# Performance work log

Hardware: AMD Instinct MI355X
Metric: run time of the kernel (lower is better)

The kernel has to match this reference:

```python
import jax, jax.numpy as jnp
import numpy as np

B, T, D, U = 32, 2048, 1024, 1024


def setup_inputs() -> dict:
    key = jax.random.key(0)
    ks = jax.random.split(key, 6)
    scale = 0.02
    return {
        "query": jax.random.normal(ks[0], (B, D), jnp.float32),
        "values": jax.random.normal(ks[1], (B, T, D), jnp.float32),
        "W1_k": jax.random.normal(ks[2], (D, U), jnp.float32) * scale,
        "W1_b": jnp.zeros((U,), jnp.float32),
        "W2_k": jax.random.normal(ks[3], (D, U), jnp.float32) * scale,
        "W2_b": jnp.zeros((U,), jnp.float32),
        "V_k": jax.random.normal(ks[4], (U, 1), jnp.float32) * scale,
        "V_b": jnp.zeros((1,), jnp.float32),
    }


def reference(query, values, W1_k, W1_b, W2_k, W2_b, V_k, V_b):
    # query: [B, D] -> [B, 1, U]; values: [B, T, D] -> [B, T, U]
    q_proj = (query @ W1_k + W1_b)[:, None, :]
    v_proj = jnp.einsum("btd,du->btu", values, W2_k) + W2_b
    # score: [B, T, 1]
    score = jnp.tanh(q_proj + v_proj) @ V_k + V_b
    attention_weights = jax.nn.softmax(score, axis=1)  # over time axis T
    context_vector = jnp.sum(attention_weights * values, axis=1)  # [B, D]
    return context_vector
```

## Files before the change

### kernel.cpp

```cpp
#include <hip/hip_runtime.h>

#define NB 32
#define NT 2048
#define ND 1024
#define NU 1024
#define NM (NB*NT)

using f32x4 = __attribute__((ext_vector_type(4))) float;
using s16x8 = __attribute__((ext_vector_type(8))) short;

#define BAR()   asm volatile("s_barrier" ::: "memory")
#define LGKM0() asm volatile("s_waitcnt lgkmcnt(0)" ::: "memory")
#define VMC(n)  asm volatile("s_waitcnt vmcnt(" #n ")" ::: "memory")

__device__ __forceinline__ unsigned short f2bf(float f) {
  unsigned u = __builtin_bit_cast(unsigned, f);
  u = u + 0x7fffu + ((u >> 16) & 1u);
  return (unsigned short)(u >> 16);
}

__device__ __forceinline__ void gload_lds16(const void* g, void* l) {
  __builtin_amdgcn_global_load_lds(
      (const __attribute__((address_space(1))) unsigned int*)g,
      (__attribute__((address_space(3))) unsigned int*)l, 16, 0, 0);
}

__device__ __forceinline__ float tanh_fast(float x) {
  float e = __expf(2.0f * x);
  return 1.0f - 2.0f * __builtin_amdgcn_rcpf(e + 1.0f);
}

__device__ __forceinline__ void stage_half(const unsigned short* g, int gk,
                                           unsigned short* l, int w, int r3, int c8s) {
#pragma unroll
  for (int i = 0; i < 2; ++i) {
    int cb = i * 8 + w;
    gload_lds16(g + (((size_t)(cb * 8 + r3)) << 10) + gk + c8s * 8, l + cb * 512);
  }
}

#define MFMA_Q(MB, NBASE) \
  _Pragma("unroll") \
  for (int m = 0; m < 4; ++m) { \
    _Pragma("unroll") \
    for (int n = 0; n < 2; ++n) { \
      _Pragma("unroll") \
      for (int ks = 0; ks < 2; ++ks) \
        acc[(MB) + m][(NBASE) + n] = __builtin_amdgcn_mfma_f32_16x16x32_bf16( \
            fa[m][ks], fb[(NBASE) + n][ks], acc[(MB) + m][(NBASE) + n], 0, 0, 0); \
    } \
  }

template<bool S1, bool S2, bool S3, bool S4, int VMN>
__device__ __forceinline__ void tile_body(
    int kt, int buf,
    const unsigned short* __restrict__ gA, const unsigned short* __restrict__ gB,
    unsigned short* sA, unsigned short* sB, f32x4 (&acc)[8][4],
    int w, int wr, int wc, int l15, int lg, int r3, int c8s) {
  const unsigned short* pA = sA + buf * 16384;
  const unsigned short* pB = sB + buf * 16384;
  const int l7 = l15 & 7;
  s16x8 fa[4][2], fb[4][2];
#pragma unroll
  for (int m = 0; m < 4; ++m)
#pragma unroll
    for (int ks = 0; ks < 2; ++ks)
      fa[m][ks] = *(const s16x8*)(pA + ((wr * 128 + m * 16 + l15) << 6) + (((ks * 4 + lg) ^ l7) << 3));
#pragma unroll
  for (int n = 0; n < 4; ++n)
#pragma unroll
    for (int ks = 0; ks < 2; ++ks)
      fb[n][ks] = *(const s16x8*)(pB + ((wc * 64 + n * 16 + l15) << 6) + (((ks * 4 + lg) ^ l7) << 3));
  if (S1) stage_half(gA + (128 << 10), (kt + 1) * 64, sA + (buf ^ 1) * 16384 + 8192, w, r3, c8s);
  BAR(); LGKM0(); __builtin_amdgcn_sched_barrier(0);
  __builtin_amdgcn_s_setprio(1);
  MFMA_Q(0, 0);
  __builtin_amdgcn_s_setprio(0);
  BAR();
  if (S2) stage_half(gB, (kt + 2) * 64, sB + buf * 16384, w, r3, c8s);
  BAR();
  __builtin_amdgcn_s_setprio(1);
  MFMA_Q(0, 2);
  __builtin_amdgcn_s_setprio(0);
  BAR();
#pragma unroll
  for (int m = 0; m < 4; ++m)
#pragma unroll
    for (int ks = 0; ks < 2; ++ks)
      fa[m][ks] = *(const s16x8*)(pA + ((wr * 128 + (4 + m) * 16 + l15) << 6) + (((ks * 4 + lg) ^ l7) << 3));
  if (S3) stage_half(gB + (128 << 10), (kt + 2) * 64, sB + buf * 16384 + 8192, w, r3, c8s);
  BAR(); LGKM0(); __builtin_amdgcn_sched_barrier(0);
  __builtin_amdgcn_s_setprio(1);
  MFMA_Q(4, 0);
  __builtin_amdgcn_s_setprio(0);
  BAR();
  if (S4) stage_half(gA, (kt + 2) * 64, sA + buf * 16384, w, r3, c8s);
  if constexpr (VMN == 6) { VMC(6); }
  else if constexpr (VMN == 0) { VMC(0); }
  BAR();
  __builtin_amdgcn_s_setprio(1);
  MFMA_Q(4, 2);
  __builtin_amdgcn_s_setprio(0);
  BAR();
}

__global__ __launch_bounds__(512, 2) void k_score_gemm8(
    const unsigned short* __restrict__ vbf, const unsigned short* __restrict__ W2t,
    const float* __restrict__ add2, const float* __restrict__ Vk,
    float* __restrict__ score_part) {
  __shared__ unsigned short sA[32768];
  __shared__ unsigned short sB[32768];
  const int tid = threadIdx.x;
  const int w = tid >> 6, lane = tid & 63;
  const int wr = w >> 2, wc = w & 3;
  const int l15 = lane & 15, lg = lane >> 4;
  const int r3 = lane >> 3, c8s = (lane & 7) ^ r3;

  const int L = blockIdx.x;
  const int g = (L & 7) * 128 + (L >> 3);
  const int mtile = g >> 2, ntile = g & 3;

  const unsigned short* gA = vbf + ((size_t)mtile << 18);
  const unsigned short* gB = W2t + ((size_t)ntile << 18);

  f32x4 acc[8][4] = {};

  stage_half(gA, 0, sA, w, r3, c8s);
  stage_half(gA + (128 << 10), 0, sA + 8192, w, r3, c8s);
  stage_half(gB, 0, sB, w, r3, c8s);
  stage_half(gB + (128 << 10), 0, sB + 8192, w, r3, c8s);
  stage_half(gB, 64, sB + 16384, w, r3, c8s);
  stage_half(gB + (128 << 10), 64, sB + 16384 + 8192, w, r3, c8s);
  stage_half(gA, 64, sA + 16384, w, r3, c8s);
  VMC(6);
  BAR();

  int buf = 0;
  for (int kt = 0; kt < 14; ++kt) {
    tile_body<true, true, true, true, 6>(kt, buf, gA, gB, sA, sB, acc, w, wr, wc, l15, lg, r3, c8s);
    buf ^= 1;
  }
  tile_body<true, false, false, false, 0>(14, buf, gA, gB, sA, sB, acc, w, wr, wc, l15, lg, r3, c8s);
  buf ^= 1;
  tile_body<false, false, false, false, -1>(15, buf, gA, gB, sA, sB, acc, w, wr, wc, l15, lg, r3, c8s);

  const int b = (mtile * 256) >> 11;
  float vks[4], adds[4];
#pragma unroll
  for (int n = 0; n < 4; ++n) {
    int u = ntile * 256 + wc * 64 + n * 16 + l15;
    vks[n] = Vk[u];
    adds[n] = add2[(b << 10) + u];
  }
  __syncthreads();
  float* part = (float*)sA;
#pragma unroll
  for (int m = 0; m < 8; ++m) {
#pragma unroll
    for (int j = 0; j < 4; ++j) {
      float s = 0.f;
#pragma unroll
      for (int n = 0; n < 4; ++n) {
        float x = acc[m][n][j] + adds[n];
        s = fmaf(tanh_fast(x), vks[n], s);
      }
#pragma unroll
      for (int off = 1; off < 16; off <<= 1) s += __shfl_xor(s, off);
      if (l15 == 0) part[wc * 256 + wr * 128 + m * 16 + lg * 4 + j] = s;
    }
  }
  __syncthreads();
  if (tid < 256) {
    float v = part[tid] + part[256 + tid] + part[512 + tid] + part[768 + tid];
    score_part[((size_t)ntile << 16) + mtile * 256 + tid] = v;
  }
}

__global__ void k_qproj(const float* __restrict__ q, const float* __restrict__ W1,
                        const float* __restrict__ W1b, const float* __restrict__ W2b,
                        float* __restrict__ add2) {
  int u = blockIdx.x * 256 + threadIdx.x;
  int b = blockIdx.y;
  const float* qr = q + (b << 10);
  float s = 0.f;
#pragma unroll 8
  for (int d = 0; d < ND; ++d) s = fmaf(qr[d], W1[d * NU + u], s);
  add2[(b << 10) + u] = s + W1b[u] + W2b[u];
}

__global__ void k_w2t(const float* __restrict__ W2, unsigned short* __restrict__ W2t) {
  __shared__ unsigned short tile[64][65];
  int bu = blockIdx.x * 64, bd = blockIdx.y * 64;
  int x = threadIdx.x & 63, y4 = threadIdx.x >> 6;
#pragma unroll
  for (int r = 0; r < 16; ++r) {
    int dl = y4 * 16 + r;
    tile[x][dl] = f2bf(W2[(size_t)(bd + dl) * NU + bu + x]);
  }
  __syncthreads();
#pragma unroll
  for (int r = 0; r < 16; ++r) {
    int ul = y4 * 16 + r;
    W2t[(size_t)(bu + ul) * ND + bd + x] = tile[ul][x];
  }
}

__global__ void k_cvt_values(const float4* __restrict__ v, ushort4* __restrict__ o) {
  const int n4 = NM * ND / 4;
  for (int i = blockIdx.x * blockDim.x + threadIdx.x; i < n4; i += gridDim.x * blockDim.x) {
    float4 f = v[i];
    ushort4 h;
    h.x = f2bf(f.x); h.y = f2bf(f.y); h.z = f2bf(f.z); h.w = f2bf(f.w);
    o[i] = h;
  }
}

__global__ __launch_bounds__(256) void k_score_gemm_small(
    const float* __restrict__ values, const unsigned short* __restrict__ W2t,
    const float* __restrict__ add2, const float* __restrict__ Vk,
    float* __restrict__ score_part) {
  __shared__ unsigned short sA[128 * 64];
  __shared__ unsigned short sB[128 * 64];
  const int tid = threadIdx.x;
  const int w = tid >> 6, lane = tid & 63;
  const int wr = w >> 1, wc = w & 1;
  const int l15 = lane & 15, lg = lane >> 4;
  const int r8 = lane >> 3, c8 = lane & 7;
  const int cs8 = c8 ^ r8;
  const int L = blockIdx.x;
  const int mtile = (L & 7) * 64 + ((L >> 3) >> 3);
  const int ntile = (L >> 3) & 7;
  f32x4 acc[4][4] = {};
  for (int kk = 0; kk < 16; ++kk) {
    const int k0 = kk * 64;
#pragma unroll
    for (int i = 0; i < 4; ++i) {
      int nl = (w * 4 + i) * 8 + r8;
      gload_lds16(W2t + ((size_t)(ntile * 128 + nl) << 10) + k0 + cs8 * 8, sB + (w * 4 + i) * 512);
    }
#pragma unroll
    for (int i = 0; i < 8; ++i) {
      int idx = tid + (i << 8);
      int row = idx >> 4, kc = idx & 15;
      const float4 f = *(const float4*)(values + ((size_t)(mtile * 128 + row) << 10) + k0 + kc * 4);
      ushort4 h;
      h.x = f2bf(f.x); h.y = f2bf(f.y); h.z = f2bf(f.z); h.w = f2bf(f.w);
      int cc = (kc >> 1) ^ (row & 7);
      *(ushort4*)(sA + (row << 6) + cc * 8 + (kc & 1) * 4) = h;
    }
    __syncthreads();
#pragma unroll
    for (int ks = 0; ks < 2; ++ks) {
      s16x8 af[4], bfr[4];
#pragma unroll
      for (int m = 0; m < 4; ++m) {
        int row = wr * 64 + m * 16 + l15;
        int cc = (ks * 4 + lg) ^ (l15 & 7);
        af[m] = *(const s16x8*)(sA + (row << 6) + cc * 8);
      }
#pragma unroll
      for (int n = 0; n < 4; ++n) {
        int row = wc * 64 + n * 16 + l15;
        int cc = (ks * 4 + lg) ^ (l15 & 7);
        bfr[n] = *(const s16x8*)(sB + (row << 6) + cc * 8);
      }
#pragma unroll
      for (int m = 0; m < 4; ++m)
#pragma unroll
        for (int n = 0; n < 4; ++n)
          acc[m][n] = __builtin_amdgcn_mfma_f32_16x16x32_bf16(af[m], bfr[n], acc[m][n], 0, 0, 0);
    }
    __syncthreads();
  }
  const int b = (mtile * 128) >> 11;
  float vks[4], adds[4];
#pragma unroll
  for (int n = 0; n < 4; ++n) {
    int u = ntile * 128 + wc * 64 + n * 16 + l15;
    vks[n] = Vk[u];
    adds[n] = add2[(b << 10) + u];
  }
  float rs[4][4];
#pragma unroll
  for (int m = 0; m < 4; ++m)
#pragma unroll
    for (int j = 0; j < 4; ++j) {
      float s = 0.f;
#pragma unroll
      for (int n = 0; n < 4; ++n) {
        float x = acc[m][n][j] + adds[n];
        s = fmaf(tanh_fast(x), vks[n], s);
      }
#pragma unroll
      for (int off = 1; off < 16; off <<= 1) s += __shfl_xor(s, off);
      rs[m][j] = s;
    }
  __syncthreads();
  float* rowsum = (float*)sA;
  if (wc == 0 && l15 == 0)
#pragma unroll
    for (int m = 0; m < 4; ++m)
#pragma unroll
      for (int j = 0; j < 4; ++j) rowsum[wr * 64 + m * 16 + lg * 4 + j] = rs[m][j];
  __syncthreads();
  if (wc == 1 && l15 == 0)
#pragma unroll
    for (int m = 0; m < 4; ++m)
#pragma unroll
      for (int j = 0; j < 4; ++j) rowsum[wr * 64 + m * 16 + lg * 4 + j] += rs[m][j];
  __syncthreads();
  if (tid < 128)
    score_part[((size_t)ntile << 16) + mtile * 128 + tid] = rowsum[tid];
}

__global__ void k_softmax(const float* __restrict__ sp, float* __restrict__ w, int npart) {
  __shared__ float redm[4], reds[4];
  int b = blockIdx.x, tid = threadIdx.x;
  float s[8];
  float mx = -1e30f;
#pragma unroll
  for (int i = 0; i < 8; ++i) {
    int t = i * 256 + tid;
    float v = 0.f;
    for (int p = 0; p < npart; ++p) v += sp[((size_t)p << 16) + (b << 11) + t];
    s[i] = v;
    mx = fmaxf(mx, v);
  }
#pragma unroll
  for (int o = 1; o < 64; o <<= 1) mx = fmaxf(mx, __shfl_xor(mx, o));
  if ((tid & 63) == 0) redm[tid >> 6] = mx;
  __syncthreads();
  mx = fmaxf(fmaxf(redm[0], redm[1]), fmaxf(redm[2], redm[3]));
  float sum = 0.f;
#pragma unroll
  for (int i = 0; i < 8; ++i) { s[i] = __expf(s[i] - mx); sum += s[i]; }
#pragma unroll
  for (int o = 1; o < 64; o <<= 1) sum += __shfl_xor(sum, o);
  if ((tid & 63) == 0) reds[tid >> 6] = sum;
  __syncthreads();
  float inv = 1.0f / (reds[0] + reds[1] + reds[2] + reds[3]);
#pragma unroll
  for (int i = 0; i < 8; ++i) w[(b << 11) + i * 256 + tid] = s[i] * inv;
}

__global__ void k_context(const float* __restrict__ values, const float* __restrict__ wv,
                          float* __restrict__ part) {
  int d = blockIdx.x * 256 + threadIdx.x;
  int b = blockIdx.y, tc = blockIdx.z;
  const float* vb = values + ((size_t)b << 21) + ((size_t)tc << 18) + d;
  const float* wb = wv + (b << 11) + (tc << 8);
  float acc = 0.f;
#pragma unroll 8
  for (int t = 0; t < 256; ++t) acc = fmaf(wb[t], vb[(size_t)t << 10], acc);
  part[(((size_t)tc * NB + b) << 10) + d] = acc;
}

__global__ void k_ctx_reduce(const float* __restrict__ part, float* __restrict__ out) {
  int i = blockIdx.x * 256 + threadIdx.x;
  float s = 0.f;
#pragma unroll
  for (int p = 0; p < 8; ++p) s += part[(p << 15) + i];
  out[i] = s;
}

extern "C" void kernel_launch(void* const* d_in, const int* in_sizes, int n_in,
                              void* d_out, int out_size, void* d_ws, size_t ws_size,
                              hipStream_t stream) {
  const float* query  = (const float*)d_in[0];
  const float* values = (const float*)d_in[1];
  const float* W1k    = (const float*)d_in[2];
  const float* W1b    = (const float*)d_in[3];
  const float* W2k    = (const float*)d_in[4];
  const float* W2b    = (const float*)d_in[5];
  const float* Vk     = (const float*)d_in[6];
  float* out = (float*)d_out;
  char* ws = (char*)d_ws;

  size_t off = 0;
  float* add2 = (float*)(ws + off); off += (size_t)NB * NU * 4;
  float* sp   = (float*)(ws + off); off += (size_t)8 * NM * 4;
  float* wv   = (float*)(ws + off); off += (size_t)NM * 4;
  float* ctxp = (float*)(ws + off); off += (size_t)8 * NB * ND * 4;
  unsigned short* W2t = (unsigned short*)(ws + off); off += (size_t)NU * ND * 2;
  unsigned short* vbf = (unsigned short*)(ws + off);
  size_t need_big = off + (size_t)NM * ND * 2;
  bool big = ws_size >= need_big;

  k_qproj<<<dim3(4, 32), 256, 0, stream>>>(query, W1k, W1b, W2b, add2);
  k_w2t<<<dim3(16, 16), 256, 0, stream>>>(W2k, W2t);
  if (big) {
    k_cvt_values<<<dim3(2048), 256, 0, stream>>>((const float4*)values, (ushort4*)vbf);
    k_score_gemm8<<<dim3(1024), 512, 0, stream>>>(vbf, W2t, add2, Vk, sp);
    k_softmax<<<dim3(32), 256, 0, stream>>>(sp, wv, 4);
  } else {
    k_score_gemm_small<<<dim3(4096), 256, 0, stream>>>(values, W2t, add2, Vk, sp);
    k_softmax<<<dim3(32), 256, 0, stream>>>(sp, wv, 8);
  }
  k_context<<<dim3(4, 32, 8), 256, 0, stream>>>(values, wv, ctxp);
  k_ctx_reduce<<<dim3(128), 256, 0, stream>>>(ctxp, out);
}
```

Baseline: 359.4 us.

## Restructure score GEMM into 4-stage K=32 pipeline and vectorize context kernel

```diff
diff --git a/kernel.cpp b/kernel.cpp
--- a/kernel.cpp
+++ b/kernel.cpp
@@ -12,6 +12,7 @@
 #define BAR()   asm volatile("s_barrier" ::: "memory")
 #define LGKM0() asm volatile("s_waitcnt lgkmcnt(0)" ::: "memory")
 #define VMC(n)  asm volatile("s_waitcnt vmcnt(" #n ")" ::: "memory")
+#define SB0()   __builtin_amdgcn_sched_barrier(0)
 
 __device__ __forceinline__ unsigned short f2bf(float f) {
   unsigned u = __builtin_bit_cast(unsigned, f);
@@ -30,81 +31,74 @@
   return 1.0f - 2.0f * __builtin_amdgcn_rcpf(e + 1.0f);
 }
 
-__device__ __forceinline__ void stage_half(const unsigned short* g, int gk,
-                                           unsigned short* l, int w, int r3, int c8s) {
+__device__ __forceinline__ void stage_tile(const unsigned short* g, unsigned short* l,
+                                           int w, int lane) {
+  int l2 = lane >> 2;
+  int gc = (lane & 3) ^ ((lane >> 3) & 3);
 #pragma unroll
   for (int i = 0; i < 2; ++i) {
-    int cb = i * 8 + w;
-    gload_lds16(g + (((size_t)(cb * 8 + r3)) << 10) + gk + c8s * 8, l + cb * 512);
-  }
-}
-
-#define MFMA_Q(MB, NBASE) \
+    int rblk = w * 2 + i;
+    int row = rblk * 16 + l2;
+    gload_lds16(g + (size_t)row * 1024 + gc * 8, l + rblk * 512);
+  }
+}
+
+__device__ __forceinline__ s16x8 frag_read(const unsigned short* buf, int row, int lg) {
+  int cr = lg ^ ((row >> 1) & 3);
+  return *(const s16x8*)(buf + row * 32 + cr * 8);
+}
+
+#define MFMA16(MB, FA) \
   _Pragma("unroll") \
   for (int m = 0; m < 4; ++m) { \
     _Pragma("unroll") \
-    for (int n = 0; n < 2; ++n) { \
-      _Pragma("unroll") \
-      for (int ks = 0; ks < 2; ++ks) \
-        acc[(MB) + m][(NBASE) + n] = __builtin_amdgcn_mfma_f32_16x16x32_bf16( \
-            fa[m][ks], fb[(NBASE) + n][ks], acc[(MB) + m][(NBASE) + n], 0, 0, 0); \
-    } \
-  }
-
-template<bool S1, bool S2, bool S3, bool S4, int VMN>
+    for (int n = 0; n < 4; ++n) \
+      acc[(MB) + m][n] = __builtin_amdgcn_mfma_f32_16x16x32_bf16( \
+          FA[m], fb[n], acc[(MB) + m][n], 0, 0, 0); \
+  }
+
+template<bool PRE, bool ST, int VM>
 __device__ __forceinline__ void tile_body(
-    int kt, int buf,
-    const unsigned short* __restrict__ gA, const unsigned short* __restrict__ gB,
+    int kt, const unsigned short* gA, const unsigned short* gB,
     unsigned short* sA, unsigned short* sB, f32x4 (&acc)[8][4],
-    int w, int wr, int wc, int l15, int lg, int r3, int c8s) {
-  const unsigned short* pA = sA + buf * 16384;
-  const unsigned short* pB = sB + buf * 16384;
-  const int l7 = l15 & 7;
-  s16x8 fa[4][2], fb[4][2];
-#pragma unroll
-  for (int m = 0; m < 4; ++m)
-#pragma unroll
-    for (int ks = 0; ks < 2; ++ks)
-      fa[m][ks] = *(const s16x8*)(pA + ((wr * 128 + m * 16 + l15) << 6) + (((ks * 4 + lg) ^ l7) << 3));
-#pragma unroll
-  for (int n = 0; n < 4; ++n)
-#pragma unroll
-    for (int ks = 0; ks < 2; ++ks)
-      fb[n][ks] = *(const s16x8*)(pB + ((wc * 64 + n * 16 + l15) << 6) + (((ks * 4 + lg) ^ l7) << 3));
-  if (S1) stage_half(gA + (128 << 10), (kt + 1) * 64, sA + (buf ^ 1) * 16384 + 8192, w, r3, c8s);
-  BAR(); LGKM0(); __builtin_amdgcn_sched_barrier(0);
+    s16x8 (&fa03)[4], s16x8 (&fa47)[4], s16x8 (&fb)[4],
+    int w, int lane, int wr, int wc, int l15, int lg) {
+  const unsigned short* pA = sA + (kt & 3) * 8192;
+  const unsigned short* qA = sA + ((kt + 1) & 3) * 8192;
+  const unsigned short* qB = sB + ((kt + 1) & 3) * 8192;
+  unsigned short* stA = sA + ((kt + 3) & 3) * 8192;
+  unsigned short* stB = sB + ((kt + 3) & 3) * 8192;
+  LGKM0(); SB0();
   __builtin_amdgcn_s_setprio(1);
-  MFMA_Q(0, 0);
+  MFMA16(0, fa03);
   __builtin_amdgcn_s_setprio(0);
+  SB0();
+#pragma unroll
+  for (int i = 0; i < 4; ++i)
+    fa47[i] = frag_read(pA, wr * 128 + (4 + i) * 16 + l15, lg);
+  if (ST) stage_tile(gA + (size_t)(kt + 3) * 32, stA, w, lane);
+  if constexpr (VM == 6) { VMC(6); }
+  else if constexpr (VM == 4) { VMC(4); }
+  else if constexpr (VM == 0) { VMC(0); }
   BAR();
-  if (S2) stage_half(gB, (kt + 2) * 64, sB + buf * 16384, w, r3, c8s);
+  LGKM0(); SB0();
+  __builtin_amdgcn_s_setprio(1);
+  MFMA16(4, fa47);
+  __builtin_amdgcn_s_setprio(0);
+  SB0();
+  if (PRE) {
+#pragma unroll
+    for (int i = 0; i < 4; ++i)
+      fa03[i] = frag_read(qA, wr * 128 + i * 16 + l15, lg);
+#pragma unroll
+    for (int n = 0; n < 4; ++n)
+      fb[n] = frag_read(qB, wc * 64 + n * 16 + l15, lg);
+  }
+  if (ST) stage_tile(gB + (size_t)(kt + 3) * 32, stB, w, lane);
   BAR();
-  __builtin_amdgcn_s_setprio(1);
-  MFMA_Q(0, 2);
-  __builtin_amdgcn_s_setprio(0);
-  BAR();
-#pragma unroll
-  for (int m = 0; m < 4; ++m)
-#pragma unroll
-    for (int ks = 0; ks < 2; ++ks)
-      fa[m][ks] = *(const s16x8*)(pA + ((wr * 128 + (4 + m) * 16 + l15) << 6) + (((ks * 4 + lg) ^ l7) << 3));
-  if (S3) stage_half(gB + (128 << 10), (kt + 2) * 64, sB + buf * 16384 + 8192, w, r3, c8s);
-  BAR(); LGKM0(); __builtin_amdgcn_sched_barrier(0);
-  __builtin_amdgcn_s_setprio(1);
-  MFMA_Q(4, 0);
-  __builtin_amdgcn_s_setprio(0);
-  BAR();
-  if (S4) stage_half(gA, (kt + 2) * 64, sA + buf * 16384, w, r3, c8s);
-  if constexpr (VMN == 6) { VMC(6); }
-  else if constexpr (VMN == 0) { VMC(0); }
-  BAR();
-  __builtin_amdgcn_s_setprio(1);
-  MFMA_Q(4, 2);
-  __builtin_amdgcn_s_setprio(0);
-  BAR();
-}
-
-__global__ __launch_bounds__(512, 2) void k_score_gemm8(
+}
+
+__global__ __launch_bounds__(512, 2) void k_score_gemm32(
     const unsigned short* __restrict__ vbf, const unsigned short* __restrict__ W2t,
     const float* __restrict__ add2, const float* __restrict__ Vk,
     float* __restrict__ score_part) {
@@ -114,7 +108,6 @@
   const int w = tid >> 6, lane = tid & 63;
   const int wr = w >> 2, wc = w & 3;
   const int l15 = lane & 15, lg = lane >> 4;
-  const int r3 = lane >> 3, c8s = (lane & 7) ^ r3;
 
   const int L = blockIdx.x;
   const int g = (L & 7) * 128 + (L >> 3);
@@ -124,25 +117,24 @@
   const unsigned short* gB = W2t + ((size_t)ntile << 18);
 
   f32x4 acc[8][4] = {};
-
-  stage_half(gA, 0, sA, w, r3, c8s);
-  stage_half(gA + (128 << 10), 0, sA + 8192, w, r3, c8s);
-  stage_half(gB, 0, sB, w, r3, c8s);
-  stage_half(gB + (128 << 10), 0, sB + 8192, w, r3, c8s);
-  stage_half(gB, 64, sB + 16384, w, r3, c8s);
-  stage_half(gB + (128 << 10), 64, sB + 16384 + 8192, w, r3, c8s);
-  stage_half(gA, 64, sA + 16384, w, r3, c8s);
-  VMC(6);
+  s16x8 fa03[4], fa47[4], fb[4];
+
+  stage_tile(gA, sA, w, lane);              stage_tile(gB, sB, w, lane);
+  stage_tile(gA + 32, sA + 8192, w, lane);  stage_tile(gB + 32, sB + 8192, w, lane);
+  stage_tile(gA + 64, sA + 16384, w, lane); stage_tile(gB + 64, sB + 16384, w, lane);
+  VMC(8);
   BAR();
-
-  int buf = 0;
-  for (int kt = 0; kt < 14; ++kt) {
-    tile_body<true, true, true, true, 6>(kt, buf, gA, gB, sA, sB, acc, w, wr, wc, l15, lg, r3, c8s);
-    buf ^= 1;
-  }
-  tile_body<true, false, false, false, 0>(14, buf, gA, gB, sA, sB, acc, w, wr, wc, l15, lg, r3, c8s);
-  buf ^= 1;
-  tile_body<false, false, false, false, -1>(15, buf, gA, gB, sA, sB, acc, w, wr, wc, l15, lg, r3, c8s);
+#pragma unroll
+  for (int i = 0; i < 4; ++i) fa03[i] = frag_read(sA, wr * 128 + i * 16 + l15, lg);
+#pragma unroll
+  for (int n = 0; n < 4; ++n) fb[n] = frag_read(sB, wc * 64 + n * 16 + l15, lg);
+
+#pragma unroll 1
+  for (int kt = 0; kt < 29; ++kt)
+    tile_body<true, true, 6>(kt, gA, gB, sA, sB, acc, fa03, fa47, fb, w, lane, wr, wc, l15, lg);
+  tile_body<true, false, 4>(29, gA, gB, sA, sB, acc, fa03, fa47, fb, w, lane, wr, wc, l15, lg);
+  tile_body<true, false, 0>(30, gA, gB, sA, sB, acc, fa03, fa47, fb, w, lane, wr, wc, l15, lg);
+  tile_body<false, false, -1>(31, gA, gB, sA, sB, acc, fa03, fa47, fb, w, lane, wr, wc, l15, lg);
 
   const int b = (mtile * 256) >> 11;
   float vks[4], adds[4];
@@ -345,14 +337,20 @@
 
 __global__ void k_context(const float* __restrict__ values, const float* __restrict__ wv,
                           float* __restrict__ part) {
-  int d = blockIdx.x * 256 + threadIdx.x;
+  int d4 = threadIdx.x;
   int b = blockIdx.y, tc = blockIdx.z;
-  const float* vb = values + ((size_t)b << 21) + ((size_t)tc << 18) + d;
+  const float4* vb = (const float4*)(values + ((size_t)b << 21) + ((size_t)tc << 18)) + d4;
   const float* wb = wv + (b << 11) + (tc << 8);
-  float acc = 0.f;
-#pragma unroll 8
-  for (int t = 0; t < 256; ++t) acc = fmaf(wb[t], vb[(size_t)t << 10], acc);
-  part[(((size_t)tc * NB + b) << 10) + d] = acc;
+  float ax = 0.f, ay = 0.f, az = 0.f, aw = 0.f;
+#pragma unroll 4
+  for (int t = 0; t < 256; ++t) {
+    float4 v = vb[(size_t)t << 8];
+    float wt = wb[t];
+    ax = fmaf(wt, v.x, ax); ay = fmaf(wt, v.y, ay);
+    az = fmaf(wt, v.z, az); aw = fmaf(wt, v.w, aw);
+  }
+  float4* po = (float4*)(part + (((size_t)tc * NB + b) << 10)) + d4;
+  *po = make_float4(ax, ay, az, aw);
 }
 
 __global__ void k_ctx_reduce(const float* __restrict__ part, float* __restrict__ out) {
@@ -390,12 +388,12 @@
   k_w2t<<<dim3(16, 16), 256, 0, stream>>>(W2k, W2t);
   if (big) {
     k_cvt_values<<<dim3(2048), 256, 0, stream>>>((const float4*)values, (ushort4*)vbf);
-    k_score_gemm8<<<dim3(1024), 512, 0, stream>>>(vbf, W2t, add2, Vk, sp);
+    k_score_gemm32<<<dim3(1024), 512, 0, stream>>>(vbf, W2t, add2, Vk, sp);
     k_softmax<<<dim3(32), 256, 0, stream>>>(sp, wv, 4);
   } else {
     k_score_gemm_small<<<dim3(4096), 256, 0, stream>>>(values, W2t, add2, Vk, sp);
     k_softmax<<<dim3(32), 256, 0, stream>>>(sp, wv, 8);
   }
-  k_context<<<dim3(4, 32, 8), 256, 0, stream>>>(values, wv, ctxp);
+  k_context<<<dim3(1, 32, 8), 256, 0, stream>>>(values, wv, ctxp);
   k_ctx_reduce<<<dim3(128), 256, 0, stream>>>(ctxp, out);
 }
```

New measurement: 351.6 us. -2.2%, faster.
